# Kernel optimization log

Measured on AMD Instinct MI355X. Metric: run time of the kernel, lower is better.

## Reference

```python
import jax, jax.numpy as jnp
import numpy as np

N_NODES = 50000
N_EDGES = 1600000
NUM_BASIS = 10
HIDDEN = 64
MAX_RADIUS = 3.0
WEIGHT_NUMEL = 5  # paths: (0x0->0),(0x1->1),(1x0->1),(1x1->0),(1x1->1)


def setup_inputs() -> dict:
    key = jax.random.key(0)
    k1, k2, k3, k4, k5 = jax.random.split(key, 5)
    f_1 = jax.random.normal(k1, (N_NODES, 4), dtype=jnp.float32)
    pos = jax.random.uniform(k2, (N_NODES, 3), dtype=jnp.float32) * MAX_RADIUS
    edge_index = jax.random.randint(k3, (2, N_EDGES), 0, N_NODES, dtype=jnp.int64)
    # radial MLP params (e3nn FullyConnectedNet init: std-normal weights)
    W1 = jax.random.normal(k4, (NUM_BASIS, HIDDEN), dtype=jnp.float32)
    W2 = jax.random.normal(k5, (HIDDEN, WEIGHT_NUMEL), dtype=jnp.float32)
    return {"f_1": f_1, "pos": pos, "W1": W1, "W2": W2, "edge_index": edge_index}


def _forward(f_1, pos, W1, W2, edge_index):
    row, col = edge_index[0], edge_index[1]
    num_nodes = f_1.shape[0]
    num_neighbors = edge_index.shape[1] / num_nodes

    edge_vec = pos[row] - pos[col]                      # [E,3]
    r2 = jnp.sum(edge_vec * edge_vec, axis=-1)
    r = jnp.sqrt(jnp.maximum(r2, 1e-12))                # [E]
    unit = edge_vec / r[:, None]

    # spherical harmonics 0e+1e, component normalization, e3nn (y,z,x) order
    sh = jnp.concatenate(
        [jnp.ones_like(unit[:, :1]), jnp.sqrt(3.0) * unit[:, [1, 2, 0]]], axis=-1
    )                                                   # [E,4]

    # soft_one_hot_linspace, basis='smooth_finite', cutoff=True
    values = jnp.linspace(0.0, MAX_RADIUS, NUM_BASIS + 2)[1:-1]
    step = values[1] - values[0]
    diff = (r[:, None] - values) / step                 # [E,num_basis]
    inside = jnp.abs(diff) < 1.0
    d = jnp.where(inside, diff, 0.0)
    C = 1.14136 * float(np.e) ** 2
    emb = jnp.where(inside, C * jnp.exp(-1.0 / (1.0 + d) - 1.0 / (1.0 - d)), 0.0)

    # e3nn FullyConnectedNet [num_basis, hidden, weight_numel] with relu
    # hidden: act normalized to unit 2nd moment (relu -> *sqrt(2)); weights /sqrt(fan_in)
    h = jax.nn.relu(emb @ (W1 / jnp.sqrt(float(NUM_BASIS)))) * jnp.sqrt(2.0)
    w = h @ (W2 / jnp.sqrt(float(HIDDEN)))              # [E,5]

    # FullyConnectedTensorProduct (0e+1e) x (0e+1e) -> (0e+1e), per-edge weights
    x = f_1[row]
    x0, xv = x[:, 0], x[:, 1:4]
    y0, yv = sh[:, 0], sh[:, 1:4]
    inv_s3 = 1.0 / jnp.sqrt(3.0)
    inv_s6 = 1.0 / jnp.sqrt(6.0)
    # output 0e: fan-in 2 paths -> norm sqrt(1/2)
    out0 = jnp.sqrt(0.5) * (
        w[:, 0] * x0 * y0 + w[:, 3] * jnp.sum(xv * yv, axis=-1) * inv_s3
    )
    # output 1e: fan-in 3 paths -> norm sqrt(3/3)=1
    outv = (
        w[:, 1:2] * x0[:, None] * yv * inv_s3
        + w[:, 2:3] * xv * y0[:, None] * inv_s3
        + w[:, 4:5] * jnp.cross(xv, yv) * inv_s6
    )
    f_edge = jnp.concatenate([out0[:, None], outv], axis=-1)  # [E,4]

    out = jax.ops.segment_sum(f_edge, col, num_segments=num_nodes)
    return out / jnp.sqrt(num_neighbors).astype(out.dtype)


def reference(f_1, pos, W1, W2, edge_index):
    return _forward(f_1, pos, W1, W2, edge_index)
```

## Files before the change

### kernel.cpp

```cpp
#include <hip/hip_runtime.h>
#include <math.h>

#define N_NODES_C 50000
#define N_EDGES_C 1600000
#define EPB3 4096
#define NBLK_E3 391
#define NBLK_N 196
#define TBL 256

#define NREG 25
#define RSH 11
#define RNODES 2048
#define CAPL 17
#define NCHG 32

#define QSCALE 1024.0f
#define QINV   (1.0f / 1024.0f)

__device__ __forceinline__ int detect_is64_block(const void* eidx, int t, int* lds_flag) {
    if (t < 64) {
        const long long* p = (const long long*)eidx;
        bool ok = true;
        for (int k = 0; k < 4; ++k) {
            long long v = p[t * 4 + k];
            ok &= (v >= 0 && v < (long long)N_NODES_C);
        }
        unsigned long long m = __ballot(ok);
        if (t == 0) *lds_flag = (m == ~0ull) ? 1 : 0;
    }
    __syncthreads();
    return *lds_flag;
}

__device__ __forceinline__ int load_col(const void* eidx, int is64, int e) {
    return is64 ? (int)((const long long*)eidx)[N_EDGES_C + e]
                : ((const int*)eidx)[N_EDGES_C + e];
}
__device__ __forceinline__ int load_row(const void* eidx, int is64, int e) {
    return is64 ? (int)((const long long*)eidx)[e]
                : ((const int*)eidx)[e];
}

__device__ __forceinline__ void edge_quant(const float* __restrict__ f1,
                                           const float* __restrict__ pos,
                                           const float* __restrict__ w1s,
                                           const float* __restrict__ W2,
                                           int row, int col, int v[4]) {
    v[0] = v[1] = v[2] = v[3] = 0;
    float px = pos[row * 3 + 0] - pos[col * 3 + 0];
    float py = pos[row * 3 + 1] - pos[col * 3 + 1];
    float pz = pos[row * 3 + 2] - pos[col * 3 + 2];
    float r2 = px * px + py * py + pz * pz;
    float r = sqrtf(fmaxf(r2, 1e-12f));
    float inv_r = 1.0f / r;
    float ux = px * inv_r, uy = py * inv_r, uz = pz * inv_r;
    const float SQ3 = 1.7320508075688772f;
    float yv0 = SQ3 * uy, yv1 = SQ3 * uz, yv2 = SQ3 * ux;

    const float C = 8.433573069075486f;
    float tt = r * (11.0f / 3.0f);
    int k1 = (int)tt;
    float d = tt - (float)k1;
    float e0 = 0.f, e1 = 0.f;
    int b0 = 0, b1 = 0;
    if (k1 >= 1 && k1 <= 10) {
        b0 = k1 - 1;
        e0 = C * __expf(-1.0f / (1.0f + d) - 1.0f / (1.0f - d));
    }
    int k2 = k1 + 1;
    if (k2 <= 10 && d > 0.f) {
        b1 = k2 - 1;
        float d2 = d - 1.0f;
        e1 = C * __expf(-1.0f / (1.0f + d2) - 1.0f / (1.0f - d2));
    }
    if (e0 == 0.f && e1 == 0.f) return;

    const float* r0 = &w1s[b0 * 68];
    const float* r1 = &w1s[b1 * 68];
    float w0 = 0.f, w1a = 0.f, w2a = 0.f, w3 = 0.f, w4 = 0.f;
#pragma unroll
    for (int j = 0; j < 64; j += 4) {
        float4 a = *(const float4*)(r0 + j);
        float4 b = *(const float4*)(r1 + j);
        float h0 = fmaxf(e0 * a.x + e1 * b.x, 0.f);
        float h1 = fmaxf(e0 * a.y + e1 * b.y, 0.f);
        float h2 = fmaxf(e0 * a.z + e1 * b.z, 0.f);
        float h3 = fmaxf(e0 * a.w + e1 * b.w, 0.f);
        w0  += h0 * W2[(j + 0) * 5 + 0] + h1 * W2[(j + 1) * 5 + 0] + h2 * W2[(j + 2) * 5 + 0] + h3 * W2[(j + 3) * 5 + 0];
        w1a += h0 * W2[(j + 0) * 5 + 1] + h1 * W2[(j + 1) * 5 + 1] + h2 * W2[(j + 2) * 5 + 1] + h3 * W2[(j + 3) * 5 + 1];
        w2a += h0 * W2[(j + 0) * 5 + 2] + h1 * W2[(j + 1) * 5 + 2] + h2 * W2[(j + 2) * 5 + 2] + h3 * W2[(j + 3) * 5 + 2];
        w3  += h0 * W2[(j + 0) * 5 + 3] + h1 * W2[(j + 1) * 5 + 3] + h2 * W2[(j + 2) * 5 + 3] + h3 * W2[(j + 3) * 5 + 3];
        w4  += h0 * W2[(j + 0) * 5 + 4] + h1 * W2[(j + 1) * 5 + 4] + h2 * W2[(j + 2) * 5 + 4] + h3 * W2[(j + 3) * 5 + 4];
    }
    const float SC = 0.05590169943749474f;
    w0 *= SC; w1a *= SC; w2a *= SC; w3 *= SC; w4 *= SC;

    float4 x = *(const float4*)(f1 + row * 4);
    float x0 = x.x, xv0 = x.y, xv1 = x.z, xv2 = x.w;

    const float INV_S3 = 0.5773502691896258f;
    const float INV_S6 = 0.4082482904638631f;
    const float SQH    = 0.7071067811865476f;
    const float INV_SQRT_NN = 0.17677669529663687f;

    float dotxy = xv0 * yv0 + xv1 * yv1 + xv2 * yv2;
    float out0 = SQH * (w0 * x0 + w3 * dotxy * INV_S3) * INV_SQRT_NN;
    float cx0 = xv1 * yv2 - xv2 * yv1;
    float cx1 = xv2 * yv0 - xv0 * yv2;
    float cx2 = xv0 * yv1 - xv1 * yv0;
    float o1 = (w1a * x0 * yv0 * INV_S3 + w2a * xv0 * INV_S3 + w4 * cx0 * INV_S6) * INV_SQRT_NN;
    float o2 = (w1a * x0 * yv1 * INV_S3 + w2a * xv1 * INV_S3 + w4 * cx1 * INV_S6) * INV_SQRT_NN;
    float o3 = (w1a * x0 * yv2 * INV_S3 + w2a * xv2 * INV_S3 + w4 * cx2 * INV_S6) * INV_SQRT_NN;

    v[0] = min(8191, max(-8191, (int)rintf(out0 * QSCALE)));
    v[1] = min(8191, max(-8191, (int)rintf(o1   * QSCALE)));
    v[2] = min(8191, max(-8191, (int)rintf(o2   * QSCALE)));
    v[3] = min(8191, max(-8191, (int)rintf(o3   * QSCALE)));
}

__device__ __forceinline__ unsigned long long edge_q(
        float prx, float pry, float prz, float4 xx,
        float pcx, float pcy, float pcz,
        const float* tC0, const float* tC1, const float* tC2,
        const float* tC3, const float* tC4) {
    float px = prx - pcx;
    float py = pry - pcy;
    float pz = prz - pcz;
    float r2 = px * px + py * py + pz * pz;
    float r = sqrtf(fmaxf(r2, 1e-12f));
    float inv_r = 1.0f / r;
    float uv0 = py * inv_r, uv1 = pz * inv_r, uv2 = px * inv_r;

    float ft = fminf(r * (255.0f / 3.0f), 255.0f);
    int idx = min((int)ft, TBL - 2);
    float fr = ft - (float)idx;
    float c0 = fmaf(fr, tC0[idx + 1] - tC0[idx], tC0[idx]);
    float c1 = fmaf(fr, tC1[idx + 1] - tC1[idx], tC1[idx]);
    float c2 = fmaf(fr, tC2[idx + 1] - tC2[idx], tC2[idx]);
    float c3 = fmaf(fr, tC3[idx + 1] - tC3[idx], tC3[idx]);
    float c4 = fmaf(fr, tC4[idx + 1] - tC4[idx], tC4[idx]);

    float x0 = xx.x, xv0 = xx.y, xv1 = xx.z, xv2 = xx.w;

    float dotxy = xv0 * uv0 + xv1 * uv1 + xv2 * uv2;
    float out0 = c0 * x0 + c3 * dotxy;
    float cx0 = xv1 * uv2 - xv2 * uv1;
    float cx1 = xv2 * uv0 - xv0 * uv2;
    float cx2 = xv0 * uv1 - xv1 * uv0;
    float c1x = c1 * x0;
    float o1 = c1x * uv0 + c2 * xv0 + c4 * cx0;
    float o2 = c1x * uv1 + c2 * xv1 + c4 * cx1;
    float o3 = c1x * uv2 + c2 * xv2 + c4 * cx2;

    int v0 = min(8191, max(-8191, (int)rintf(out0 * QSCALE)));
    int v1 = min(8191, max(-8191, (int)rintf(o1 * QSCALE)));
    int v2 = min(8191, max(-8191, (int)rintf(o2 * QSCALE)));
    int v3 = min(8191, max(-8191, (int)rintf(o3 * QSCALE)));

    return (unsigned long long)((long long)v0 + ((long long)v1 << 16)
         + ((long long)v2 << 32) + ((long long)v3 << 48));
}

__global__ __launch_bounds__(1024)
void binscatter_kernel(const float* __restrict__ f1, const float* __restrict__ pos,
                       const float* __restrict__ W1, const float* __restrict__ W2,
                       const void* __restrict__ eidx,
                       unsigned* __restrict__ gOff,
                       unsigned* __restrict__ rcG,
                       float* __restrict__ nodeq,
                       float* __restrict__ tG) {
    __shared__ unsigned rcbuf[EPB3];
    __shared__ unsigned stageRc[EPB3];
    __shared__ unsigned histB[4][32];
    __shared__ unsigned gBaseS[32];
    __shared__ unsigned localBaseS[32];
    __shared__ unsigned cursorLocS[32];
    __shared__ int flag_s;
    const int t = threadIdx.x;
    float* w1s = (float*)stageRc;
    if (blockIdx.x == 0) {
        for (int i = t; i < 640; i += 1024) w1s[(i >> 6) * 68 + (i & 63)] = W1[i];
    }
    if (t < 128) histB[t >> 5][t & 31] = 0u;
    const int is64 = detect_is64_block(eidx, t, &flag_s);

    if (blockIdx.x == 0 && t < TBL) {
        float tt = (float)t * (11.0f / 255.0f);
        int k1 = (int)tt;
        float d = tt - (float)k1;
        const float C = 8.433573069075486f;
        float e0 = 0.f, e1 = 0.f;
        int b0 = 0, b1 = 0;
        if (k1 >= 1 && k1 <= 10) {
            b0 = k1 - 1;
            e0 = C * __expf(-1.0f / (1.0f + d) - 1.0f / (1.0f - d));
        }
        int k2 = k1 + 1;
        if (k2 <= 10 && d > 0.f) {
            b1 = k2 - 1;
            float d2 = d - 1.0f;
            e1 = C * __expf(-1.0f / (1.0f + d2) - 1.0f / (1.0f - d2));
        }
        float w0 = 0.f, w1 = 0.f, w2 = 0.f, w3 = 0.f, w4 = 0.f;
        const float* r0 = &w1s[b0 * 68];
        const float* r1 = &w1s[b1 * 68];
#pragma unroll
        for (int j = 0; j < 64; j += 4) {
            float4 a = *(const float4*)(r0 + j);
            float4 b = *(const float4*)(r1 + j);
            float h0 = fmaxf(e0 * a.x + e1 * b.x, 0.f);
            float h1 = fmaxf(e0 * a.y + e1 * b.y, 0.f);
            float h2 = fmaxf(e0 * a.z + e1 * b.z, 0.f);
            float h3 = fmaxf(e0 * a.w + e1 * b.w, 0.f);
            w0 += h0 * W2[(j + 0) * 5 + 0] + h1 * W2[(j + 1) * 5 + 0] + h2 * W2[(j + 2) * 5 + 0] + h3 * W2[(j + 3) * 5 + 0];
            w1 += h0 * W2[(j + 0) * 5 + 1] + h1 * W2[(j + 1) * 5 + 1] + h2 * W2[(j + 2) * 5 + 1] + h3 * W2[(j + 3) * 5 + 1];
            w2 += h0 * W2[(j + 0) * 5 + 2] + h1 * W2[(j + 1) * 5 + 2] + h2 * W2[(j + 2) * 5 + 2] + h3 * W2[(j + 3) * 5 + 2];
            w3 += h0 * W2[(j + 0) * 5 + 3] + h1 * W2[(j + 1) * 5 + 3] + h2 * W2[(j + 2) * 5 + 3] + h3 * W2[(j + 3) * 5 + 3];
            w4 += h0 * W2[(j + 0) * 5 + 4] + h1 * W2[(j + 1) * 5 + 4] + h2 * W2[(j + 2) * 5 + 4] + h3 * W2[(j + 3) * 5 + 4];
        }
        const float SC  = 0.05590169943749474f;
        const float ISN = 0.17677669529663687f;
        const float SQH = 0.7071067811865476f;
        const float INV_S3 = 0.5773502691896258f;
        const float INV_S6 = 0.4082482904638631f;
        const float SQ3 = 1.7320508075688772f;
        float base = SC * ISN;
        tG[0 * TBL + t] = SQH * base * w0;
        tG[1 * TBL + t] = base * w1;
        tG[2 * TBL + t] = INV_S3 * base * w2;
        tG[3 * TBL + t] = SQH * base * w3;
        tG[4 * TBL + t] = INV_S6 * SQ3 * base * w4;
    }

    const int e0b = blockIdx.x * EPB3;
    const int nedge = min(EPB3, N_EDGES_C - e0b);
    const int hb = (t >> 6) & 3;
    for (int i = t; i < nedge; i += 1024) {
        int row = load_row(eidx, is64, e0b + i);
        int col = load_col(eidx, is64, e0b + i);
        rcbuf[i] = ((unsigned)row << 16) | (unsigned)col;
        atomicAdd(&histB[hb][col >> RSH], 1u);
    }
    {
        int n = blockIdx.x * 1024 + t;
        if (n < N_NODES_C) {
            float4 f = *(const float4*)(f1 + 4 * n);
            float4 p;
            p.x = pos[3 * n + 0];
            p.y = pos[3 * n + 1];
            p.z = pos[3 * n + 2];
            p.w = 0.f;
            *(float4*)(nodeq + 8 * n)     = p;
            *(float4*)(nodeq + 8 * n + 4) = f;
        }
    }
    __syncthreads();
    if (t == 0) {
        unsigned run = 0u;
        for (int b = 0; b < 32; ++b) {
            localBaseS[b] = run;
            cursorLocS[b] = run;
            run += histB[0][b] + histB[1][b] + histB[2][b] + histB[3][b];
        }
    }
    if (t < 32) {
        unsigned h = histB[0][t] + histB[1][t] + histB[2][t] + histB[3][t];
        gBaseS[t] = ((unsigned)t << CAPL) + atomicAdd(&gOff[t], h);
    }
    __syncthreads();
    for (int i = t; i < nedge; i += 1024) {
        unsigned rc = rcbuf[i];
        int b = (int)((rc & 0xFFFFu) >> RSH);
        unsigned p = atomicAdd(&cursorLocS[b], 1u);
        stageRc[p] = rc;
    }
    __syncthreads();
    for (int i = t; i < nedge; i += 1024) {
        unsigned rc = stageRc[i];
        int b = (int)((rc & 0xFFFFu) >> RSH);
        unsigned dst = gBaseS[b] + ((unsigned)i - localBaseS[b]);
        unsigned lim = ((unsigned)(b + 1)) << CAPL;
        if (dst < lim) rcG[dst] = rc;
    }
}

__global__ __launch_bounds__(512)
void mgather_kernel(const unsigned* __restrict__ rcG,
                    const unsigned* __restrict__ gOff,
                    const float* __restrict__ pos,
                    const float* __restrict__ nodeq,
                    const float* __restrict__ tG,
                    unsigned long long* __restrict__ acc) {
    __shared__ unsigned long long accs[RNODES];
    __shared__ float posx[RNODES];
    __shared__ float posy[RNODES];
    __shared__ float posz[RNODES];
    __shared__ float tC0[TBL];
    __shared__ float tC1[TBL];
    __shared__ float tC2[TBL];
    __shared__ float tC3[TBL];
    __shared__ float tC4[TBL];
    const int t = threadIdx.x;
    const int B = blockIdx.x;
    const int c = blockIdx.y;
    if (t < TBL) {
        tC0[t] = tG[0 * TBL + t];
        tC1[t] = tG[1 * TBL + t];
        tC2[t] = tG[2 * TBL + t];
        tC3[t] = tG[3 * TBL + t];
        tC4[t] = tG[4 * TBL + t];
    }
    const int nb0 = B << RSH;
    for (int j = t; j < RNODES; j += 512) {
        accs[j] = 0ull;
        int n = nb0 + j;
        if (n < N_NODES_C) {
            posx[j] = pos[3 * n + 0];
            posy[j] = pos[3 * n + 1];
            posz[j] = pos[3 * n + 2];
        }
    }
    __syncthreads();

    unsigned cnt = min(gOff[B], (unsigned)(1u << CAPL));
    unsigned i0 = (unsigned)(((unsigned long long)cnt * (unsigned)c) / NCHG);
    unsigned i1 = (unsigned)(((unsigned long long)cnt * (unsigned)(c + 1)) / NCHG);
    const unsigned* src = rcG + ((size_t)B << CAPL);

    unsigned i = i0 + t;
    for (; i + 512 < i1; i += 1024) {
        unsigned rcA = src[i];
        unsigned rcB = src[i + 512];
        int rowA = (int)(rcA >> 16), lcA = (int)(rcA & (RNODES - 1));
        int rowB = (int)(rcB >> 16), lcB = (int)(rcB & (RNODES - 1));
        const float4* nrA = (const float4*)(nodeq + ((size_t)rowA << 3));
        const float4* nrB = (const float4*)(nodeq + ((size_t)rowB << 3));
        float4 prA = nrA[0];
        float4 xxA = nrA[1];
        float4 prB = nrB[0];
        float4 xxB = nrB[1];
        float pcxA = posx[lcA], pcyA = posy[lcA], pczA = posz[lcA];
        float pcxB = posx[lcB], pcyB = posy[lcB], pczB = posz[lcB];
        unsigned long long QA = edge_q(prA.x, prA.y, prA.z, xxA, pcxA, pcyA, pczA,
                                       tC0, tC1, tC2, tC3, tC4);
        unsigned long long QB = edge_q(prB.x, prB.y, prB.z, xxB, pcxB, pcyB, pczB,
                                       tC0, tC1, tC2, tC3, tC4);
        atomicAdd(&accs[lcA], QA);
        atomicAdd(&accs[lcB], QB);
    }
    for (; i < i1; i += 512) {
        unsigned rc = src[i];
        int row = (int)(rc >> 16), lc = (int)(rc & (RNODES - 1));
        const float4* nr = (const float4*)(nodeq + ((size_t)row << 3));
        float4 pr = nr[0];
        float4 xx = nr[1];
        unsigned long long Q = edge_q(pr.x, pr.y, pr.z, xx, posx[lc], posy[lc], posz[lc],
                                      tC0, tC1, tC2, tC3, tC4);
        atomicAdd(&accs[lc], Q);
    }
    __syncthreads();
    for (int j = t; j < RNODES; j += 512) {
        unsigned long long v = accs[j];
        int n = nb0 + j;
        if (v && n < N_NODES_C) {
            __hip_atomic_fetch_add(acc + n, v, __ATOMIC_RELAXED, __HIP_MEMORY_SCOPE_AGENT);
        }
    }
}

__global__ __launch_bounds__(256)
void reduce_unpack(const unsigned long long* __restrict__ acc, float* __restrict__ out) {
    int n = blockIdx.x * 256 + threadIdx.x;
    if (n >= N_NODES_C) return;
    long long T = (long long)acc[n];
    int s0 = (int)(short)(T & 0xFFFF); T = (T - s0) >> 16;
    int s1 = (int)(short)(T & 0xFFFF); T = (T - s1) >> 16;
    int s2 = (int)(short)(T & 0xFFFF); T = (T - s2) >> 16;
    int s3 = (int)T;
    float4 o;
    o.x = (float)s0 * QINV; o.y = (float)s1 * QINV;
    o.z = (float)s2 * QINV; o.w = (float)s3 * QINV;
    *(float4*)(out + 4 * n) = o;
}

__global__ __launch_bounds__(256)
void init_acc(unsigned long long* __restrict__ acc,
              const void* __restrict__ eidx, int* __restrict__ flag) {
    int i = blockIdx.x * 256 + threadIdx.x;
    if (i < N_NODES_C) acc[i] = 0ull;
    if (blockIdx.x == 0 && threadIdx.x < 64) {
        const long long* p = (const long long*)eidx;
        bool ok = true;
        for (int k = 0; k < 4; ++k) {
            long long v = p[threadIdx.x * 4 + k];
            ok &= (v >= 0 && v < (long long)N_NODES_C);
        }
        unsigned long long m = __ballot(ok);
        if (threadIdx.x == 0) *flag = (m == ~0ull) ? 1 : 0;
    }
}

__global__ __launch_bounds__(256)
void equi_conv_atomic(const float* __restrict__ f1, const float* __restrict__ pos,
                      const float* __restrict__ W1, const float* __restrict__ W2,
                      const void* __restrict__ eidx, const int* __restrict__ flag_p,
                      unsigned long long* __restrict__ acc) {
    __shared__ float w1s[10 * 68];
    const int tid = threadIdx.x;
    for (int i = tid; i < 640; i += 256) w1s[(i >> 6) * 68 + (i & 63)] = W1[i];
    __syncthreads();
    const int e = blockIdx.x * 256 + tid;
    if (e >= N_EDGES_C) return;
    const int is64 = *flag_p;
    int row = load_row(eidx, is64, e);
    int col = load_col(eidx, is64, e);
    int v[4];
    edge_quant(f1, pos, w1s, W2, row, col, v);
    if (v[0] | v[1] | v[2] | v[3]) {
        unsigned long long P = (unsigned long long)((long long)v[0] + ((long long)v[1] << 16)
                             + ((long long)v[2] << 32) + ((long long)v[3] << 48));
        __hip_atomic_fetch_add(acc + col, P, __ATOMIC_RELAXED, __HIP_MEMORY_SCOPE_AGENT);
    }
}

extern "C" void kernel_launch(void* const* d_in, const int* in_sizes, int n_in,
                              void* d_out, int out_size, void* d_ws, size_t ws_size,
                              hipStream_t stream) {
    const float* f1  = (const float*)d_in[0];
    const float* pos = (const float*)d_in[1];
    const float* W1  = (const float*)d_in[2];
    const float* W2  = (const float*)d_in[3];
    const void*  eix = d_in[4];
    float* out = (float*)d_out;

    const size_t offRC = 0;
    const size_t szRC  = ((size_t)32 << CAPL) * 4;
    const size_t offC  = offRC + szRC;
    const size_t szC   = 32 * 4;
    const size_t offA  = offC + szC;
    const size_t szA   = (size_t)N_NODES_C * 8;
    const size_t offT  = (offA + szA + 15) & ~(size_t)15;
    const size_t szT   = (size_t)5 * TBL * 4;
    const size_t offQ  = (offT + szT + 15) & ~(size_t)15;
    const size_t szQ   = (size_t)N_NODES_C * 32;
    const size_t need  = offQ + szQ;

    if (ws_size >= need) {
        unsigned*           rcG   = (unsigned*)((char*)d_ws + offRC);
        unsigned*           gOff  = (unsigned*)((char*)d_ws + offC);
        unsigned long long* acc   = (unsigned long long*)((char*)d_ws + offA);
        float*              tG    = (float*)((char*)d_ws + offT);
        float*              nodeq = (float*)((char*)d_ws + offQ);

        hipMemsetAsync(gOff, 0, szC + szA, stream);
        binscatter_kernel<<<NBLK_E3, 1024, 0, stream>>>(f1, pos, W1, W2, eix, gOff, rcG, nodeq, tG);
        mgather_kernel<<<dim3(NREG, NCHG), 512, 0, stream>>>(rcG, gOff, pos, nodeq, tG, acc);
        reduce_unpack<<<NBLK_N, 256, 0, stream>>>(acc, out);
    } else {
        unsigned long long* acc = (unsigned long long*)d_ws;
        int* flag = (int*)((char*)d_ws + (size_t)N_NODES_C * 8);
        const int nblk = (N_NODES_C + 255) / 256;
        init_acc<<<nblk, 256, 0, stream>>>(acc, eix, flag);
        equi_conv_atomic<<<(N_EDGES_C + 255) / 256, 256, 0, stream>>>(f1, pos, W1, W2, eix, flag, acc);
        reduce_unpack<<<nblk, 256, 0, stream>>>(acc, out);
    }
}
```

Measured before the change: 103.8 us.

## Use smaller 1024-node regions with 256-thread gather blocks and 4-way unrolling

Halves the destination-node region size from 2048 to 1024 nodes, which doubles the number of regions to 49 and the histogram bins to 64 in the binning kernel. The gather kernel now runs 256-thread blocks over 49x16 blocks, uses a smaller LDS footprint per block, and unrolls the edge loop 4-way with predicated tails. The aim is to raise occupancy and memory-level parallelism in the gather and reduce LDS pressure. The cost is more bins in the scatter, more global flushes of per-region accumulators, and per-region capacity shrinking to 65536 edges (about 32768 expected per region).

```diff
diff --git a/kernel.cpp b/kernel.cpp
--- a/kernel.cpp
+++ b/kernel.cpp
@@ -8,11 +8,12 @@
 #define NBLK_N 196
 #define TBL 256
 
-#define NREG 25
-#define RSH 11
-#define RNODES 2048
-#define CAPL 17
-#define NCHG 32
+#define NREG 49
+#define NREGP 64
+#define RSH 10
+#define RNODES 1024
+#define CAPL 16
+#define NCHG 16
 
 #define QSCALE 1024.0f
 #define QINV   (1.0f / 1024.0f)
@@ -171,17 +172,17 @@
                        float* __restrict__ tG) {
     __shared__ unsigned rcbuf[EPB3];
     __shared__ unsigned stageRc[EPB3];
-    __shared__ unsigned histB[4][32];
-    __shared__ unsigned gBaseS[32];
-    __shared__ unsigned localBaseS[32];
-    __shared__ unsigned cursorLocS[32];
+    __shared__ unsigned histB[4][NREGP];
+    __shared__ unsigned gBaseS[NREGP];
+    __shared__ unsigned localBaseS[NREGP];
+    __shared__ unsigned cursorLocS[NREGP];
     __shared__ int flag_s;
     const int t = threadIdx.x;
     float* w1s = (float*)stageRc;
     if (blockIdx.x == 0) {
         for (int i = t; i < 640; i += 1024) w1s[(i >> 6) * 68 + (i & 63)] = W1[i];
     }
-    if (t < 128) histB[t >> 5][t & 31] = 0u;
+    if (t < 256) histB[t >> 6][t & 63] = 0u;
     const int is64 = detect_is64_block(eidx, t, &flag_s);
 
     if (blockIdx.x == 0 && t < TBL) {
@@ -257,13 +258,13 @@
     __syncthreads();
     if (t == 0) {
         unsigned run = 0u;
-        for (int b = 0; b < 32; ++b) {
+        for (int b = 0; b < NREGP; ++b) {
             localBaseS[b] = run;
             cursorLocS[b] = run;
             run += histB[0][b] + histB[1][b] + histB[2][b] + histB[3][b];
         }
     }
-    if (t < 32) {
+    if (t < NREGP) {
         unsigned h = histB[0][t] + histB[1][t] + histB[2][t] + histB[3][t];
         gBaseS[t] = ((unsigned)t << CAPL) + atomicAdd(&gOff[t], h);
     }
@@ -284,7 +285,7 @@
     }
 }
 
-__global__ __launch_bounds__(512)
+__global__ __launch_bounds__(256)
 void mgather_kernel(const unsigned* __restrict__ rcG,
                     const unsigned* __restrict__ gOff,
                     const float* __restrict__ pos,
@@ -303,15 +304,13 @@
     const int t = threadIdx.x;
     const int B = blockIdx.x;
     const int c = blockIdx.y;
-    if (t < TBL) {
-        tC0[t] = tG[0 * TBL + t];
-        tC1[t] = tG[1 * TBL + t];
-        tC2[t] = tG[2 * TBL + t];
-        tC3[t] = tG[3 * TBL + t];
-        tC4[t] = tG[4 * TBL + t];
-    }
+    tC0[t] = tG[0 * TBL + t];
+    tC1[t] = tG[1 * TBL + t];
+    tC2[t] = tG[2 * TBL + t];
+    tC3[t] = tG[3 * TBL + t];
+    tC4[t] = tG[4 * TBL + t];
     const int nb0 = B << RSH;
-    for (int j = t; j < RNODES; j += 512) {
+    for (int j = t; j < RNODES; j += 256) {
         accs[j] = 0ull;
         int n = nb0 + j;
         if (n < N_NODES_C) {
@@ -327,39 +326,41 @@
     unsigned i1 = (unsigned)(((unsigned long long)cnt * (unsigned)(c + 1)) / NCHG);
     const unsigned* src = rcG + ((size_t)B << CAPL);
 
-    unsigned i = i0 + t;
-    for (; i + 512 < i1; i += 1024) {
-        unsigned rcA = src[i];
-        unsigned rcB = src[i + 512];
-        int rowA = (int)(rcA >> 16), lcA = (int)(rcA & (RNODES - 1));
-        int rowB = (int)(rcB >> 16), lcB = (int)(rcB & (RNODES - 1));
-        const float4* nrA = (const float4*)(nodeq + ((size_t)rowA << 3));
-        const float4* nrB = (const float4*)(nodeq + ((size_t)rowB << 3));
-        float4 prA = nrA[0];
-        float4 xxA = nrA[1];
-        float4 prB = nrB[0];
-        float4 xxB = nrB[1];
-        float pcxA = posx[lcA], pcyA = posy[lcA], pczA = posz[lcA];
-        float pcxB = posx[lcB], pcyB = posy[lcB], pczB = posz[lcB];
-        unsigned long long QA = edge_q(prA.x, prA.y, prA.z, xxA, pcxA, pcyA, pczA,
+    for (unsigned ib = i0 + t; ib < i1; ib += 1024) {
+        unsigned ia = ib + 256, ic = ib + 512, id = ib + 768;
+        bool va = ia < i1, vb = ic < i1, vc = id < i1;
+        unsigned rc0 = src[ib];
+        unsigned rc1 = va ? src[ia] : rc0;
+        unsigned rc2 = vb ? src[ic] : rc0;
+        unsigned rc3 = vc ? src[id] : rc0;
+        int row0 = (int)(rc0 >> 16), lc0 = (int)(rc0 & (RNODES - 1));
+        int row1 = (int)(rc1 >> 16), lc1 = (int)(rc1 & (RNODES - 1));
+        int row2 = (int)(rc2 >> 16), lc2 = (int)(rc2 & (RNODES - 1));
+        int row3 = (int)(rc3 >> 16), lc3 = (int)(rc3 & (RNODES - 1));
+        const float4* nr0 = (const float4*)(nodeq + ((size_t)row0 << 3));
+        const float4* nr1 = (const float4*)(nodeq + ((size_t)row1 << 3));
+        const float4* nr2 = (const float4*)(nodeq + ((size_t)row2 << 3));
+        const float4* nr3 = (const float4*)(nodeq + ((size_t)row3 << 3));
+        float4 pr0 = nr0[0], xx0 = nr0[1];
+        float4 pr1 = nr1[0], xx1 = nr1[1];
+        float4 pr2 = nr2[0], xx2 = nr2[1];
+        float4 pr3 = nr3[0], xx3 = nr3[1];
+
+        unsigned long long Q0 = edge_q(pr0.x, pr0.y, pr0.z, xx0, posx[lc0], posy[lc0], posz[lc0],
                                        tC0, tC1, tC2, tC3, tC4);
-        unsigned long long QB = edge_q(prB.x, prB.y, prB.z, xxB, pcxB, pcyB, pczB,
+        unsigned long long Q1 = edge_q(pr1.x, pr1.y, pr1.z, xx1, posx[lc1], posy[lc1], posz[lc1],
                                        tC0, tC1, tC2, tC3, tC4);
-        atomicAdd(&accs[lcA], QA);
-        atomicAdd(&accs[lcB], QB);
-    }
-    for (; i < i1; i += 512) {
-        unsigned rc = src[i];
-        int row = (int)(rc >> 16), lc = (int)(rc & (RNODES - 1));
-        const float4* nr = (const float4*)(nodeq + ((size_t)row << 3));
-        float4 pr = nr[0];
-        float4 xx = nr[1];
-        unsigned long long Q = edge_q(pr.x, pr.y, pr.z, xx, posx[lc], posy[lc], posz[lc],
-                                      tC0, tC1, tC2, tC3, tC4);
-        atomicAdd(&accs[lc], Q);
-    }
-    __syncthreads();
-    for (int j = t; j < RNODES; j += 512) {
+        unsigned long long Q2 = edge_q(pr2.x, pr2.y, pr2.z, xx2, posx[lc2], posy[lc2], posz[lc2],
+                                       tC0, tC1, tC2, tC3, tC4);
+        unsigned long long Q3 = edge_q(pr3.x, pr3.y, pr3.z, xx3, posx[lc3], posy[lc3], posz[lc3],
+                                       tC0, tC1, tC2, tC3, tC4);
+        atomicAdd(&accs[lc0], Q0);
+        if (va) atomicAdd(&accs[lc1], Q1);
+        if (vb) atomicAdd(&accs[lc2], Q2);
+        if (vc) atomicAdd(&accs[lc3], Q3);
+    }
+    __syncthreads();
+    for (int j = t; j < RNODES; j += 256) {
         unsigned long long v = accs[j];
         int n = nb0 + j;
         if (v && n < N_NODES_C) {
@@ -434,9 +435,9 @@
     float* out = (float*)d_out;
 
     const size_t offRC = 0;
-    const size_t szRC  = ((size_t)32 << CAPL) * 4;
+    const size_t szRC  = ((size_t)NREGP << CAPL) * 4;
     const size_t offC  = offRC + szRC;
-    const size_t szC   = 32 * 4;
+    const size_t szC   = NREGP * 4;
     const size_t offA  = offC + szC;
     const size_t szA   = (size_t)N_NODES_C * 8;
     const size_t offT  = (offA + szA + 15) & ~(size_t)15;
@@ -454,7 +455,7 @@
 
         hipMemsetAsync(gOff, 0, szC + szA, stream);
         binscatter_kernel<<<NBLK_E3, 1024, 0, stream>>>(f1, pos, W1, W2, eix, gOff, rcG, nodeq, tG);
-        mgather_kernel<<<dim3(NREG, NCHG), 512, 0, stream>>>(rcG, gOff, pos, nodeq, tG, acc);
+        mgather_kernel<<<dim3(NREG, NCHG), 256, 0, stream>>>(rcG, gOff, pos, nodeq, tG, acc);
         reduce_unpack<<<NBLK_N, 256, 0, stream>>>(acc, out);
     } else {
         unsigned long long* acc = (unsigned long long*)d_ws;
```

After: 104.1 us. No clear change (+0.3%).
